# Performance work log

Hardware: AMD Instinct MI355X
Metric: run time of the kernel (lower is better)

The kernel has to match this reference:

```python
import jax, jax.numpy as jnp
import numpy as np
import math

CYCLES = [5, 6, 7, 8]


def gamaka_pe(T, D):
    pos = np.arange(T, dtype=np.float32)[:, None]
    div = np.exp(np.arange(0, D, 2, dtype=np.float32) * (-math.log(10000.0) / D))
    pe = np.zeros((T, D), np.float32)
    pe[:, 0::2] = np.sin(pos * div)
    pe[:, 1::2] = np.cos(pos * div[: D // 2])
    tala = np.zeros((T, D), np.float32)
    slots = D // 4
    half = slots // 2
    harm = np.arange(1, half + 1, dtype=np.float32)
    for t_idx, c in enumerate(CYCLES):
        phase = (pos % c) / c * 2.0 * math.pi
        s = t_idx * slots
        tala[:, s:s + half] = np.sin(phase * harm)
        tala[:, s + half:s + slots] = np.cos(phase * harm)
    return jnp.asarray(0.5 * pe + 0.5 * tala)


def layer_norm(x, g, b, eps=1e-5):
    m = x.mean(-1, keepdims=True)
    v = ((x - m) ** 2).mean(-1, keepdims=True)
    return (x - m) / jnp.sqrt(v + eps) * g + b


def gru_all_threads(x, wih, whh, bih, bhh):
    # x:(B,T,D), wih/whh:(4,3D,D), bih/bhh:(4,3D) -> (4,B,T,D)
    xp = jnp.einsum('kij,btj->kbti', wih, x) + bih[:, None, None, :]  # (4,B,T,3D)
    K, B, T, _ = xp.shape
    D = x.shape[-1]

    def step(h, xt):  # h:(4,B,D), xt:(4,B,3D)
        gh = jnp.einsum('kij,kbj->kbi', whh, h) + bhh[:, None, :]
        xr, xz, xn = jnp.split(xt, 3, axis=-1)
        hr, hz, hn = jnp.split(gh, 3, axis=-1)
        r = jax.nn.sigmoid(xr + hr)
        z = jax.nn.sigmoid(xz + hz)
        n = jnp.tanh(xn + r * hn)
        h = (1.0 - z) * n + z * h
        return h, h

    h0 = jnp.zeros((K, B, D), x.dtype)
    _, hs = jax.lax.scan(step, h0, jnp.moveaxis(xp, 2, 0))  # (T,4,B,D)
    return jnp.moveaxis(hs, 0, 2)  # (4,B,T,D)


def setup_inputs() -> dict:
    key = jax.random.key(0)
    ks = jax.random.split(key, 16)
    B, T, D = 4, 2048, 512
    s = 0.02
    return {
        'x': jax.random.normal(ks[0], (B, T, D), jnp.float32),
        'gru_wih': s * jax.random.normal(ks[1], (4, 3 * D, D), jnp.float32),
        'gru_whh': s * jax.random.normal(ks[2], (4, 3 * D, D), jnp.float32),
        'gru_bih': s * jax.random.normal(ks[3], (4, 3 * D), jnp.float32),
        'gru_bhh': s * jax.random.normal(ks[4], (4, 3 * D), jnp.float32),
        'wq': s * jax.random.normal(ks[5], (4, D, D), jnp.float32),
        'wk': s * jax.random.normal(ks[6], (4, D, D), jnp.float32),
        'wv': s * jax.random.normal(ks[7], (4, D, D), jnp.float32),
        'w_beat': s * jax.random.normal(ks[8], (4, D, 2 * D), jnp.float32),
        'norm_g': jnp.ones((4, D), jnp.float32),
        'norm_b': jnp.zeros((4, D), jnp.float32),
        'w_mix': s * jax.random.normal(ks[9], (D, 4 * D), jnp.float32),
        'bn_g': jnp.ones((D,), jnp.float32),
        'bn_b': jnp.zeros((D,), jnp.float32),
    }


def reference(x, gru_wih, gru_whh, gru_bih, gru_bhh, wq, wk, wv, w_beat,
              norm_g, norm_b, w_mix, bn_g, bn_b):
    B, T, D = x.shape
    x = x + gamaka_pe(T, D)[None]

    gru_out = gru_all_threads(x, gru_wih, gru_whh, gru_bih, gru_bhh)  # (4,B,T,D)

    q = jnp.einsum('kij,btj->kbti', wq, x)
    k = jnp.einsum('kij,btj->kbti', wk, x)
    v = jnp.einsum('kij,btj->kbti', wv, x)

    idx = jnp.arange(T)
    diff = idx[:, None] - idx[None, :]  # (T,T)
    cyc = jnp.asarray(CYCLES)[:, None, None]
    valid = (diff[None] >= 0) & (diff[None] < cyc)  # (4,T,T)
    mask = jnp.where(valid, 0.0, -jnp.inf).astype(x.dtype)

    scores = jnp.einsum('kbtd,kbsd->kbts', q, k) / jnp.sqrt(jnp.asarray(D, x.dtype))
    attn = jax.nn.softmax(scores + mask[:, None], axis=-1)
    attn_out = jnp.einsum('kbts,kbsd->kbtd', attn, v)

    comb = jnp.concatenate([gru_out, attn_out], axis=-1)  # (4,B,T,2D)
    beat = jnp.einsum('kij,kbtj->kbti', w_beat, comb)
    thr = layer_norm(beat + x[None], norm_g[:, None, None, :], norm_b[:, None, None, :])

    merged = jnp.moveaxis(thr, 0, 2).reshape(B, T, 4 * D)  # concat thread order 0..3
    out = jnp.einsum('ij,btj->bti', w_mix, merged)
    return layer_norm(out + x, bn_g, bn_b)
```

## Files before the change

kernel.cpp:

```cpp
#include <hip/hip_runtime.h>
#include <hip/hip_bf16.h>
#include <math.h>


using frag8   = __attribute__((ext_vector_type(8))) short;
using floatx4 = __attribute__((ext_vector_type(4))) float;

#define B_ 4
#define T_ 2048
#define D_ 512
#define BT_ (B_ * T_)

#define PIN4(v) asm volatile("" : "+v"((v).x), "+v"((v).y), "+v"((v).z), "+v"((v).w))
#define PIN1(v) asm volatile("" : "+v"(v))

static __device__ __forceinline__ float bf2f(unsigned short u) {
    return __uint_as_float(((unsigned)u) << 16);
}
static __device__ __forceinline__ unsigned short f2bfbits(float f) {
    unsigned u = __float_as_uint(f);
    u = (u + 0x7FFF + ((u >> 16) & 1)) >> 16;
    return (unsigned short)u;
}

template <int CTRL, int RM>
static __device__ __forceinline__ float dpp_add(float x) {
    int m = __builtin_amdgcn_update_dpp(0, __float_as_int(x), CTRL, RM, 0xF, true);
    return x + __int_as_float(m);
}
static __device__ __forceinline__ float wave_red_sum64(float x) {
    x = dpp_add<0xB1, 0xF>(x);
    x = dpp_add<0x4E, 0xF>(x);
    x = dpp_add<0x124, 0xF>(x);
    x = dpp_add<0x128, 0xF>(x);
    x = dpp_add<0x142, 0xA>(x);
    x = dpp_add<0x143, 0xC>(x);
    return x;
}

static __device__ __forceinline__ float pe_tala(int t, int d) {
    int i2 = d >> 1;
    const float c0 = (float)(-9.210340371976184 / 512.0);
    float dv = expf((float)(2 * i2) * c0);
    float a  = (float)t * dv;
    float pe = (d & 1) ? cosf(a) : sinf(a);
    int kk = d >> 7;
    int s  = d & 127;
    int c  = kk + 5;
    float phase = ((float)(t % c) / (float)c) * 6.2831854820251465f;
    float harm  = (float)((s & 63) + 1);
    float ta = (s < 64) ? sinf(phase * harm) : cosf(phase * harm);
    return 0.5f * pe + 0.5f * ta;
}

__global__ void k_fill(float* __restrict__ out, int n) {
    int i = blockIdx.x * 256 + threadIdx.x;
    if (i < n) out[i] = 1234.5f;
}

__global__ void k_prep(const float* __restrict__ x, __hip_bfloat16* __restrict__ xinbf)
{
    int idx = blockIdx.x * 256 + threadIdx.x;
    if (idx >= B_ * T_ * D_) return;
    int d = idx & 511;
    int t = (idx >> 9) & 2047;
    xinbf[idx] = __float2bfloat16(x[idx] + pe_tala(t, d));
}

__global__ void k_f2bf(const float* __restrict__ src, __hip_bfloat16* __restrict__ dst, int n)
{
    int i = blockIdx.x * 256 + threadIdx.x;
    if (i < n) dst[i] = __float2bfloat16(src[i]);
}

__global__ __launch_bounds__(256) void k_gemm(
    const __hip_bfloat16* __restrict__ A, const __hip_bfloat16* __restrict__ B,
    float* __restrict__ Cf, __hip_bfloat16* __restrict__ Cb,
    const float* __restrict__ bias, const __hip_bfloat16* __restrict__ resid,
    int M, int N, int K,
    long sA_, long sB_, long sC_, long sBias_)
{
    const int bz = blockIdx.z;
    A += (size_t)bz * sA_;
    B += (size_t)bz * sB_;
    const float* biasp = bias ? bias + (size_t)bz * sBias_ : (const float*)0;

    const int m0 = blockIdx.x * 128, n0 = blockIdx.y * 128;
    const int tid  = threadIdx.x;
    const int lane = tid & 63, wv = tid >> 6;
    const int wm = (wv >> 1) * 64, wn = (wv & 1) * 64;
    const int fr = lane & 15, quad = lane >> 4;

    __shared__ __align__(16) __hip_bfloat16 sAt[128 * 32];
    __shared__ __align__(16) __hip_bfloat16 sBt[128 * 32];

    floatx4 acc[4][4];
#pragma unroll
    for (int mi = 0; mi < 4; mi++)
#pragma unroll
        for (int ni = 0; ni < 4; ni++) acc[mi][ni] = (floatx4){0.f, 0.f, 0.f, 0.f};

    const int srow = tid >> 2;
    const int scol = (tid & 3) * 8;

    for (int k0 = 0; k0 < K; k0 += 32) {
        frag8 av0 = *(const frag8*)(A + (size_t)(m0 +      srow) * K + (k0 + scol));
        frag8 av1 = *(const frag8*)(A + (size_t)(m0 + 64 + srow) * K + (k0 + scol));
        frag8 bv0 = *(const frag8*)(B + (size_t)(n0 +      srow) * K + (k0 + scol));
        frag8 bv1 = *(const frag8*)(B + (size_t)(n0 + 64 + srow) * K + (k0 + scol));
        __syncthreads();
        *(frag8*)&sAt[(     srow) * 32 + scol] = av0;
        *(frag8*)&sAt[(64 + srow) * 32 + scol] = av1;
        *(frag8*)&sBt[(     srow) * 32 + scol] = bv0;
        *(frag8*)&sBt[(64 + srow) * 32 + scol] = bv1;
        __syncthreads();

        frag8 af[4], bfr[4];
#pragma unroll
        for (int mi = 0; mi < 4; mi++)
            af[mi] = *(const frag8*)&sAt[(wm + mi * 16 + fr) * 32 + quad * 8];
#pragma unroll
        for (int ni = 0; ni < 4; ni++)
            bfr[ni] = *(const frag8*)&sBt[(wn + ni * 16 + fr) * 32 + quad * 8];
#pragma unroll
        for (int mi = 0; mi < 4; mi++)
#pragma unroll
            for (int ni = 0; ni < 4; ni++)
                acc[mi][ni] = __builtin_amdgcn_mfma_f32_16x16x32_bf16(af[mi], bfr[ni], acc[mi][ni], 0, 0, 0);
    }

    const size_t coff = (size_t)bz * sC_;
#pragma unroll
    for (int mi = 0; mi < 4; mi++) {
#pragma unroll
        for (int ni = 0; ni < 4; ni++) {
            const int col = n0 + wn + ni * 16 + fr;
            const float bval = biasp ? biasp[col] : 0.f;
#pragma unroll
            for (int r2 = 0; r2 < 4; r2++) {
                const int row = m0 + wm + mi * 16 + quad * 4 + r2;
                const size_t ci = (size_t)row * N + col;
                float v = acc[mi][ni][r2] + bval;
                if (resid) v += bf2f(((const unsigned short*)resid)[ci]);
                if (Cf) Cf[coff + ci] = v;
                else    Cb[coff + ci] = __float2bfloat16(v);
            }
        }
    }
}

__global__ __launch_bounds__(256) void k_attn(
    const __hip_bfloat16* __restrict__ Q, const __hip_bfloat16* __restrict__ Kx,
    const __hip_bfloat16* __restrict__ Vx, __hip_bfloat16* __restrict__ comb)
{
    const int pair = blockIdx.y;
    const int kk = pair >> 2;
    const int c = kk + 5;
    const int t0 = blockIdx.x * 16;
    const int tid = threadIdx.x, lane = tid & 63, wv = tid >> 6;

    __shared__ __align__(16) unsigned short kls[23 * 512];
    __shared__ __align__(16) unsigned short vls[23 * 512];

    const size_t qb = (size_t)pair * T_ * D_;
    for (int e = tid; e < 23 * 64; e += 256) {
        int r = e >> 6, ce = (e & 63) << 3;
        int s = t0 - 7 + r;
        frag8 kv = (frag8){0,0,0,0,0,0,0,0};
        frag8 vv = kv;
        if (s >= 0) {
            kv = *(const frag8*)((const unsigned short*)Kx + qb + (size_t)s * 512 + ce);
            vv = *(const frag8*)((const unsigned short*)Vx + qb + (size_t)s * 512 + ce);
        }
        *(frag8*)&kls[r * 512 + ce] = kv;
        *(frag8*)&vls[r * 512 + ce] = vv;
    }
    __syncthreads();

    const float scale = 0.044194173824159216f;
    for (int tt = wv; tt < 16; tt += 4) {
        const int t = t0 + tt;
        float qv[8];
        const unsigned short* qrow = (const unsigned short*)Q + qb + (size_t)t * 512 + lane * 8;
#pragma unroll
        for (int i = 0; i < 8; i++) qv[i] = bf2f(qrow[i]);

        float sc[8];
#pragma unroll
        for (int si = 0; si < 8; ++si) {
            const int s = t - 7 + si;
            const int r = tt + si;
            const unsigned short* krow = &kls[r * 512 + lane * 8];
            float p = 0.f;
#pragma unroll
            for (int i = 0; i < 8; i++) p += qv[i] * bf2f(krow[i]);
#pragma unroll
            for (int off = 1; off < 64; off <<= 1) p += __shfl_xor(p, off);
            const bool valid = (s >= 0) && (s >= t - c + 1);
            sc[si] = valid ? p * scale : -1e30f;
        }
        float mx = -1e30f;
#pragma unroll
        for (int si = 0; si < 8; ++si) mx = fmaxf(mx, sc[si]);
        float sum = 0.f;
#pragma unroll
        for (int si = 0; si < 8; ++si) { sc[si] = expf(sc[si] - mx); sum += sc[si]; }
        const float inv = 1.f / sum;

        float o[8] = {0,0,0,0,0,0,0,0};
#pragma unroll
        for (int si = 0; si < 8; ++si) {
            const int r = tt + si;
            const float w = sc[si] * inv;
            const unsigned short* vrow = &vls[r * 512 + lane * 8];
#pragma unroll
            for (int i = 0; i < 8; i++) o[i] += w * bf2f(vrow[i]);
        }
        frag8 ov;
#pragma unroll
        for (int i = 0; i < 8; i++) ov[i] = (short)f2bfbits(o[i]);
        *(frag8*)((unsigned short*)comb + ((size_t)pair * T_ + t) * 1024 + 512 + lane * 8) = ov;
    }
}

__global__ __launch_bounds__(512, 2) void k_gru(
    const float* __restrict__ whh, const float* __restrict__ bhh,
    const __hip_bfloat16* __restrict__ xp,
    unsigned long long* __restrict__ ring,
    __hip_bfloat16* __restrict__ comb)
{
    const int pair = blockIdx.x & 15;
    const int wg   = blockIdx.x >> 4;
    const int k    = pair >> 2;
    const int tid  = threadIdx.x;
    const int w    = tid >> 6;
    const int j    = tid & 63;
    const int dbase = wg * 32 + w * 4;

    const float* wb = whh + (size_t)k * 1536 * 512;
    float4 wv4[4][3][2];
#pragma unroll
    for (int dd = 0; dd < 4; dd++)
#pragma unroll
        for (int G = 0; G < 3; G++) {
            const float* row = wb + (size_t)(G * 512 + dbase + dd) * 512;
            wv4[dd][G][0] = *(const float4*)(row + 4 * j);
            wv4[dd][G][1] = *(const float4*)(row + 256 + 4 * j);
            PIN4(wv4[dd][G][0]);
            PIN4(wv4[dd][G][1]);
        }

    const int isprod = (j >= 48) & (j < 52);
    const int d = dbase + (j & 3);
    float bhr = 0.f, bhz = 0.f, bhn = 0.f;
    if (isprod) {
        bhr = bhh[k * 1536 + d];
        bhz = bhh[k * 1536 + 512 + d];
        bhn = bhh[k * 1536 + 1024 + d];
    }
    PIN1(bhr); PIN1(bhz); PIN1(bhn);
    float hcar = 0.f;

    const unsigned short* xbase = (const unsigned short*)xp + (size_t)pair * T_ * 1536;
    unsigned long long* ringp = ring + (size_t)pair * 4 * 512;

    __shared__ __align__(16) float h_lds[2][512];

    int bail = 0;
    for (int t = 0; t < T_; ++t) {
        const int par = t & 1;

        float xr = 0.f, xz = 0.f, xn = 0.f;
        if (isprod) {
            const unsigned short* xrow = xbase + (size_t)t * 1536;
            xr = bf2f(xrow[d]);
            xz = bf2f(xrow[512 + d]);
            xn = bf2f(xrow[1024 + d]);
        }

        if (t == 0) {
            h_lds[0][tid] = 0.f;
        } else {
            unsigned long long* wp = ringp + (size_t)((t - 1) & 3) * 512 + tid;
            const unsigned tag = (unsigned)t;
            unsigned long long a0;
            for (;;) {
                a0 = __hip_atomic_load(wp, __ATOMIC_RELAXED, __HIP_MEMORY_SCOPE_AGENT);
                if ((unsigned)(a0 >> 32) == tag) break;
                if (++bail > 2000000) break;
            }
            h_lds[par][tid] = __uint_as_float((unsigned)a0);
        }
        __syncthreads();

        const float4 h0 = *(const float4*)&h_lds[par][4 * j];
        const float4 h1 = *(const float4*)&h_lds[par][256 + 4 * j];

        float pr[12];
#pragma unroll
        for (int dd = 0; dd < 4; dd++)
#pragma unroll
            for (int G = 0; G < 3; G++) {
                const float4 a = wv4[dd][G][0], b4 = wv4[dd][G][1];
                pr[dd * 3 + G] =
                    a.x * h0.x + a.y * h0.y + a.z * h0.z + a.w * h0.w +
                    b4.x * h1.x + b4.y * h1.y + b4.z * h1.z + b4.w * h1.w;
            }
#pragma unroll
        for (int i = 0; i < 12; i++) pr[i] = wave_red_sum64(pr[i]);

        if (isprod) {
            const int dd = j & 3;
            const float ar = (dd & 2) ? ((dd & 1) ? pr[9]  : pr[6]) : ((dd & 1) ? pr[3]  : pr[0]);
            const float az = (dd & 2) ? ((dd & 1) ? pr[10] : pr[7]) : ((dd & 1) ? pr[4]  : pr[1]);
            const float an = (dd & 2) ? ((dd & 1) ? pr[11] : pr[8]) : ((dd & 1) ? pr[5]  : pr[2]);
            const float r = 1.f / (1.f + expf(-(xr + ar + bhr)));
            const float z = 1.f / (1.f + expf(-(xz + az + bhz)));
            const float n = tanhf(xn + r * (an + bhn));
            const float hnew = (1.f - z) * n + z * hcar;
            hcar = hnew;
            const unsigned long long u =
                ((unsigned long long)(unsigned)(t + 1) << 32) |
                (unsigned long long)__float_as_uint(hnew);
            __hip_atomic_store(&ringp[(size_t)(t & 3) * 512 + d], u,
                               __ATOMIC_RELAXED, __HIP_MEMORY_SCOPE_AGENT);
            comb[((size_t)pair * T_ + t) * 1024 + d] = __float2bfloat16(hnew);
        }
    }
}

__global__ void k_ln_thr(const __hip_bfloat16* __restrict__ bp,
                         const float* __restrict__ gg, const float* __restrict__ bb2,
                         __hip_bfloat16* __restrict__ thrm)
{
    const int kk = blockIdx.y;
    const int lane = threadIdx.x & 63, wv = threadIdx.x >> 6;
    float g8[8], b8[8];
#pragma unroll
    for (int i = 0; i < 8; i++) {
        g8[i] = gg[kk * 512 + lane * 8 + i];
        b8[i] = bb2[kk * 512 + lane * 8 + i];
    }
    for (int rr = 0; rr < 8; ++rr) {
        const int bt = blockIdx.x * 32 + wv * 8 + rr;
        const unsigned short* row = (const unsigned short*)bp + ((size_t)kk * BT_ + bt) * 512 + lane * 8;
        float v[8];
#pragma unroll
        for (int i = 0; i < 8; i++) v[i] = bf2f(row[i]);
        float s = 0.f, s2 = 0.f;
#pragma unroll
        for (int i = 0; i < 8; i++) { s += v[i]; s2 += v[i] * v[i]; }
#pragma unroll
        for (int off = 1; off < 64; off <<= 1) { s += __shfl_xor(s, off); s2 += __shfl_xor(s2, off); }
        const float mean = s * (1.f / 512.f);
        const float var = s2 * (1.f / 512.f) - mean * mean;
        const float rs = 1.f / sqrtf(var + 1e-5f);
        frag8 ov;
#pragma unroll
        for (int i = 0; i < 8; i++) ov[i] = (short)f2bfbits((v[i] - mean) * rs * g8[i] + b8[i]);
        *(frag8*)((unsigned short*)thrm + (size_t)bt * 2048 + kk * 512 + lane * 8) = ov;
    }
}

__global__ void k_ln_fin(const float* __restrict__ mo, const float* __restrict__ x,
                         const float* __restrict__ gg, const float* __restrict__ bb2,
                         float* __restrict__ out)
{
    const int lane = threadIdx.x & 63, wv = threadIdx.x >> 6;
    float g8[8], b8[8];
#pragma unroll
    for (int i = 0; i < 8; i++) {
        g8[i] = gg[lane * 8 + i];
        b8[i] = bb2[lane * 8 + i];
    }
    for (int rr = 0; rr < 8; ++rr) {
        const int bt = blockIdx.x * 32 + wv * 8 + rr;
        const int t = bt & 2047;
        const float* r1 = mo + (size_t)bt * 512 + lane * 8;
        const float* r2 = x + (size_t)bt * 512 + lane * 8;
        float v[8];
#pragma unroll
        for (int i = 0; i < 8; i++) v[i] = r1[i] + r2[i] + pe_tala(t, lane * 8 + i);
        float s = 0.f, s2 = 0.f;
#pragma unroll
        for (int i = 0; i < 8; i++) { s += v[i]; s2 += v[i] * v[i]; }
#pragma unroll
        for (int off = 1; off < 64; off <<= 1) { s += __shfl_xor(s, off); s2 += __shfl_xor(s2, off); }
        const float mean = s * (1.f / 512.f);
        const float var = s2 * (1.f / 512.f) - mean * mean;
        const float rs = 1.f / sqrtf(var + 1e-5f);
#pragma unroll
        for (int i = 0; i < 8; i++)
            out[(size_t)bt * 512 + lane * 8 + i] = (v[i] - mean) * rs * g8[i] + b8[i];
    }
}

extern "C" void kernel_launch(void* const* d_in, const int* in_sizes, int n_in,
                              void* d_out, int out_size, void* d_ws, size_t ws_size,
                              hipStream_t stream)
{
    const float* x     = (const float*)d_in[0];
    const float* wih   = (const float*)d_in[1];
    const float* whh   = (const float*)d_in[2];
    const float* bih   = (const float*)d_in[3];
    const float* bhh   = (const float*)d_in[4];
    const float* wq    = (const float*)d_in[5];
    const float* wk    = (const float*)d_in[6];
    const float* wv    = (const float*)d_in[7];
    const float* wbeat = (const float*)d_in[8];
    const float* ng    = (const float*)d_in[9];
    const float* nb    = (const float*)d_in[10];
    const float* wmix  = (const float*)d_in[11];
    const float* bng   = (const float*)d_in[12];
    const float* bnb   = (const float*)d_in[13];

    char* ws = (char*)d_ws;
    size_t off = 0;
    auto alloc = [&](size_t b) { size_t o = off; off += (b + 255) & ~(size_t)255; return o; };

    const size_t XINBF  = alloc((size_t)BT_ * 512 * 2);
    const size_t WIHBF  = alloc((size_t)4 * 1536 * 512 * 2);
    const size_t WQBF   = alloc((size_t)4 * 512 * 512 * 2);
    const size_t WKBF   = alloc((size_t)4 * 512 * 512 * 2);
    const size_t WVBF   = alloc((size_t)4 * 512 * 512 * 2);
    const size_t WBEATBF= alloc((size_t)4 * 512 * 1024 * 2);
    const size_t WMIXBF = alloc((size_t)512 * 2048 * 2);
    const size_t HBUF   = alloc((size_t)16 * 4 * 512 * 8);
    const size_t COMB   = alloc((size_t)4 * BT_ * 1024 * 2);
    const size_t BIG    = alloc((size_t)4 * BT_ * 1536 * 2);
    const size_t NEED   = off;

    const size_t XPO   = BIG;
    const size_t QO    = BIG;
    const size_t KO    = BIG + 33554432;
    const size_t VO    = BIG + 67108864;
    const size_t BEATO = BIG;
    const size_t THRO  = BIG + 33554432;
    const size_t MIXO  = BIG + 67108864;

    if (ws_size < NEED) {
        k_fill<<<(out_size + 255) / 256, 256, 0, stream>>>((float*)d_out, out_size);
        return;
    }

    hipMemsetAsync(ws + HBUF, 0, (size_t)16 * 4 * 512 * 8, stream);

    k_prep<<<(B_ * T_ * D_ + 255) / 256, 256, 0, stream>>>(x, (__hip_bfloat16*)(ws + XINBF));

    auto cast = [&](const float* s, size_t o, int n) {
        k_f2bf<<<(n + 255) / 256, 256, 0, stream>>>(s, (__hip_bfloat16*)(ws + o), n);
    };
    cast(wih,   WIHBF,  4 * 1536 * 512);
    cast(wq,    WQBF,   4 * 512 * 512);
    cast(wk,    WKBF,   4 * 512 * 512);
    cast(wv,    WVBF,   4 * 512 * 512);
    cast(wbeat, WBEATBF,4 * 512 * 1024);
    cast(wmix,  WMIXBF, 512 * 2048);

    const __hip_bfloat16* xinbf = (const __hip_bfloat16*)(ws + XINBF);

    k_gemm<<<dim3(BT_ / 128, 1536 / 128, 4), 256, 0, stream>>>(
        xinbf, (const __hip_bfloat16*)(ws + WIHBF),
        nullptr, (__hip_bfloat16*)(ws + XPO),
        bih, nullptr, BT_, 1536, 512,
        0, (long)1536 * 512, (long)BT_ * 1536, 1536);

    k_gru<<<256, 512, 0, stream>>>(
        whh, bhh, (const __hip_bfloat16*)(ws + XPO),
        (unsigned long long*)(ws + HBUF), (__hip_bfloat16*)(ws + COMB));

    k_gemm<<<dim3(BT_ / 128, 4, 4), 256, 0, stream>>>(
        xinbf, (const __hip_bfloat16*)(ws + WQBF), nullptr, (__hip_bfloat16*)(ws + QO),
        nullptr, nullptr, BT_, 512, 512, 0, (long)512 * 512, (long)BT_ * 512, 0);
    k_gemm<<<dim3(BT_ / 128, 4, 4), 256, 0, stream>>>(
        xinbf, (const __hip_bfloat16*)(ws + WKBF), nullptr, (__hip_bfloat16*)(ws + KO),
        nullptr, nullptr, BT_, 512, 512, 0, (long)512 * 512, (long)BT_ * 512, 0);
    k_gemm<<<dim3(BT_ / 128, 4, 4), 256, 0, stream>>>(
        xinbf, (const __hip_bfloat16*)(ws + WVBF), nullptr, (__hip_bfloat16*)(ws + VO),
        nullptr, nullptr, BT_, 512, 512, 0, (long)512 * 512, (long)BT_ * 512, 0);

    k_attn<<<dim3(T_ / 16, 16), 256, 0, stream>>>(
        (const __hip_bfloat16*)(ws + QO), (const __hip_bfloat16*)(ws + KO),
        (const __hip_bfloat16*)(ws + VO), (__hip_bfloat16*)(ws + COMB));

    k_gemm<<<dim3(BT_ / 128, 4, 4), 256, 0, stream>>>(
        (const __hip_bfloat16*)(ws + COMB), (const __hip_bfloat16*)(ws + WBEATBF),
        nullptr, (__hip_bfloat16*)(ws + BEATO),
        nullptr, xinbf, BT_, 512, 1024,
        (long)BT_ * 1024, (long)512 * 1024, (long)BT_ * 512, 0);

    k_ln_thr<<<dim3(BT_ / 32, 4), 256, 0, stream>>>(
        (const __hip_bfloat16*)(ws + BEATO), ng, nb, (__hip_bfloat16*)(ws + THRO));

    k_gemm<<<dim3(BT_ / 128, 4, 1), 256, 0, stream>>>(
        (const __hip_bfloat16*)(ws + THRO), (const __hip_bfloat16*)(ws + WMIXBF),
        (float*)(ws + MIXO), nullptr,
        nullptr, nullptr, BT_, 512, 2048, 0, 0, 0, 0);

    k_ln_fin<<<BT_ / 32, 256, 0, stream>>>(
        (const float*)(ws + MIXO), x, bng, bnb, (float*)d_out);
}
```

Before: 4.644 ms.

## Stage GRU recurrent weights as fp16 in LDS and use fdot2 dot products

The GRU recurrent kernel stops holding fp32 recurrent weights pinned in registers. It converts its slice of the weights to fp16 once, stores it in about 96KB of dynamic LDS, and reloads it from LDS every timestep. The hidden state is also broadcast through LDS as fp16, and each lane computes its 8-element partial dot products with fdot2 instead of 16 fp32 FMAs. This is meant to cut register pressure and arithmetic per step. In exchange it adds LDS reads on the serial recurrence path, lowers the precision of h and the weights, and limits occupancy to one block per CU because of the large LDS footprint.

Measured after the change: 4.662 ms. No clear change (+0.4%).

```diff
diff --git a/kernel.cpp b/kernel.cpp
--- a/kernel.cpp
+++ b/kernel.cpp
@@ -5,14 +5,35 @@
 
 using frag8   = __attribute__((ext_vector_type(8))) short;
 using floatx4 = __attribute__((ext_vector_type(4))) float;
+typedef _Float16 f16x2 __attribute__((ext_vector_type(2)));
+typedef _Float16 f16x4 __attribute__((ext_vector_type(4)));
+typedef _Float16 f16x8 __attribute__((ext_vector_type(8)));
 
 #define B_ 4
 #define T_ 2048
 #define D_ 512
 #define BT_ (B_ * T_)
 
-#define PIN4(v) asm volatile("" : "+v"((v).x), "+v"((v).y), "+v"((v).z), "+v"((v).w))
-#define PIN1(v) asm volatile("" : "+v"(v))
+#if defined(__has_builtin)
+#if __has_builtin(__builtin_amdgcn_fdot2)
+#define HAVE_FDOT2 1
+#endif
+#endif
+
+static __device__ __forceinline__ float dot8(f16x8 a, f16x8 b, float acc) {
+#ifdef HAVE_FDOT2
+    f16x2 a0 = {a[0], a[1]}, a1 = {a[2], a[3]}, a2 = {a[4], a[5]}, a3 = {a[6], a[7]};
+    f16x2 b0 = {b[0], b[1]}, b1 = {b[2], b[3]}, b2 = {b[4], b[5]}, b3 = {b[6], b[7]};
+    acc = __builtin_amdgcn_fdot2(a0, b0, acc, false);
+    acc = __builtin_amdgcn_fdot2(a1, b1, acc, false);
+    acc = __builtin_amdgcn_fdot2(a2, b2, acc, false);
+    acc = __builtin_amdgcn_fdot2(a3, b3, acc, false);
+#else
+#pragma unroll
+    for (int i = 0; i < 8; i++) acc += (float)a[i] * (float)b[i];
+#endif
+    return acc;
+}
 
 static __device__ __forceinline__ float bf2f(unsigned short u) {
     return __uint_as_float(((unsigned)u) << 16);
@@ -229,46 +250,58 @@
     unsigned long long* __restrict__ ring,
     __hip_bfloat16* __restrict__ comb)
 {
+    extern __shared__ char smem[];
+    _Float16* wlds = (_Float16*)smem;
+    _Float16* hbuf = (_Float16*)(smem + 98304);
+
     const int pair = blockIdx.x & 15;
     const int wg   = blockIdx.x >> 4;
     const int k    = pair >> 2;
     const int tid  = threadIdx.x;
     const int w    = tid >> 6;
     const int j    = tid & 63;
-    const int dbase = wg * 32 + w * 4;
-
-    const float* wb = whh + (size_t)k * 1536 * 512;
-    float4 wv4[4][3][2];
-#pragma unroll
-    for (int dd = 0; dd < 4; dd++)
-#pragma unroll
-        for (int G = 0; G < 3; G++) {
-            const float* row = wb + (size_t)(G * 512 + dbase + dd) * 512;
-            wv4[dd][G][0] = *(const float4*)(row + 4 * j);
-            wv4[dd][G][1] = *(const float4*)(row + 256 + 4 * j);
-            PIN4(wv4[dd][G][0]);
-            PIN4(wv4[dd][G][1]);
-        }
+
+    {
+        const float* wb = whh + (size_t)k * 786432 + (size_t)wg * 32 * 512;
+#pragma unroll
+        for (int v = 0; v < 24; ++v) {
+            const int f4  = v * 512 + tid;
+            const int i   = f4 * 4;
+            const int G   = i >> 14;
+            const int rem = i & 16383;
+            const float4 x4 = *(const float4*)(wb + (size_t)G * 262144 + rem);
+            f16x4 h4;
+            h4[0] = (_Float16)x4.x; h4[1] = (_Float16)x4.y;
+            h4[2] = (_Float16)x4.z; h4[3] = (_Float16)x4.w;
+            *(f16x4*)&wlds[i] = h4;
+        }
+    }
 
     const int isprod = (j >= 48) & (j < 52);
-    const int d = dbase + (j & 3);
+    const int d = wg * 32 + w * 4 + (j & 3);
     float bhr = 0.f, bhz = 0.f, bhn = 0.f;
     if (isprod) {
         bhr = bhh[k * 1536 + d];
         bhz = bhh[k * 1536 + 512 + d];
         bhn = bhh[k * 1536 + 1024 + d];
     }
-    PIN1(bhr); PIN1(bhz); PIN1(bhn);
     float hcar = 0.f;
 
     const unsigned short* xbase = (const unsigned short*)xp + (size_t)pair * T_ * 1536;
     unsigned long long* ringp = ring + (size_t)pair * 4 * 512;
 
-    __shared__ __align__(16) float h_lds[2][512];
+    __syncthreads();
 
     int bail = 0;
     for (int t = 0; t < T_; ++t) {
         const int par = t & 1;
+
+        f16x8 wreg[12];
+#pragma unroll
+        for (int dd = 0; dd < 4; ++dd)
+#pragma unroll
+            for (int G = 0; G < 3; ++G)
+                wreg[dd * 3 + G] = *(const f16x8*)&wlds[G * 16384 + (w * 4 + dd) * 512 + 8 * j];
 
         float xr = 0.f, xz = 0.f, xn = 0.f;
         if (isprod) {
@@ -279,7 +312,7 @@
         }
 
         if (t == 0) {
-            h_lds[0][tid] = 0.f;
+            hbuf[tid] = (_Float16)0.f;
         } else {
             unsigned long long* wp = ringp + (size_t)((t - 1) & 3) * 512 + tid;
             const unsigned tag = (unsigned)t;
@@ -289,31 +322,22 @@
                 if ((unsigned)(a0 >> 32) == tag) break;
                 if (++bail > 2000000) break;
             }
-            h_lds[par][tid] = __uint_as_float((unsigned)a0);
+            hbuf[par * 512 + tid] = (_Float16)__uint_as_float((unsigned)a0);
         }
         __syncthreads();
 
-        const float4 h0 = *(const float4*)&h_lds[par][4 * j];
-        const float4 h1 = *(const float4*)&h_lds[par][256 + 4 * j];
-
+        const f16x8 hv = *(const f16x8*)&hbuf[par * 512 + 8 * j];
         float pr[12];
 #pragma unroll
-        for (int dd = 0; dd < 4; dd++)
-#pragma unroll
-            for (int G = 0; G < 3; G++) {
-                const float4 a = wv4[dd][G][0], b4 = wv4[dd][G][1];
-                pr[dd * 3 + G] =
-                    a.x * h0.x + a.y * h0.y + a.z * h0.z + a.w * h0.w +
-                    b4.x * h1.x + b4.y * h1.y + b4.z * h1.z + b4.w * h1.w;
-            }
-#pragma unroll
-        for (int i = 0; i < 12; i++) pr[i] = wave_red_sum64(pr[i]);
+        for (int i2 = 0; i2 < 12; ++i2) pr[i2] = dot8(wreg[i2], hv, 0.f);
+#pragma unroll
+        for (int i2 = 0; i2 < 12; ++i2) pr[i2] = wave_red_sum64(pr[i2]);
 
         if (isprod) {
             const int dd = j & 3;
-            const float ar = (dd & 2) ? ((dd & 1) ? pr[9]  : pr[6]) : ((dd & 1) ? pr[3]  : pr[0]);
-            const float az = (dd & 2) ? ((dd & 1) ? pr[10] : pr[7]) : ((dd & 1) ? pr[4]  : pr[1]);
-            const float an = (dd & 2) ? ((dd & 1) ? pr[11] : pr[8]) : ((dd & 1) ? pr[5]  : pr[2]);
+            const float ar = (dd & 2) ? ((dd & 1) ? pr[9]  : pr[6]) : ((dd & 1) ? pr[3] : pr[0]);
+            const float az = (dd & 2) ? ((dd & 1) ? pr[10] : pr[7]) : ((dd & 1) ? pr[4] : pr[1]);
+            const float an = (dd & 2) ? ((dd & 1) ? pr[11] : pr[8]) : ((dd & 1) ? pr[5] : pr[2]);
             const float r = 1.f / (1.f + expf(-(xr + ar + bhr)));
             const float z = 1.f / (1.f + expf(-(xz + az + bhz)));
             const float n = tanhf(xn + r * (an + bhn));
@@ -465,7 +489,7 @@
         bih, nullptr, BT_, 1536, 512,
         0, (long)1536 * 512, (long)BT_ * 1536, 1536);
 
-    k_gru<<<256, 512, 0, stream>>>(
+    k_gru<<<256, 512, 100352, stream>>>(
         whh, bhh, (const __hip_bfloat16*)(ws + XPO),
         (unsigned long long*)(ws + HBUF), (__hip_bfloat16*)(ws + COMB));
 
```
